# Optimization experiments

Measured on AMD Instinct MI355X. Metric: run time of the kernel, lower is better.

## Reference

```python
import jax, jax.numpy as jnp
import numpy as np

NUM_HEADS = 4
OUTPUT_DIM = 64


def setup_inputs() -> dict:
    key = jax.random.key(0)
    k1, k2, k3 = jax.random.split(key, 3)
    B, N, F = 8, 2048, 256
    features = jax.random.normal(k1, (B, N, F), dtype=jnp.float32)
    adj_matrix = jax.random.uniform(k2, (B, N, N), dtype=jnp.float32)
    # learned params (glorot-ish scale)
    kernel = jax.random.normal(k3, (F, OUTPUT_DIM * NUM_HEADS), dtype=jnp.float32) * (1.0 / np.sqrt(F))
    bias = jnp.zeros((OUTPUT_DIM * NUM_HEADS,), dtype=jnp.float32)
    return {"features": features, "adj_matrix": adj_matrix, "kernel": kernel, "bias": bias}


def reference(features, adj_matrix, kernel, bias):
    B, N, F = features.shape
    H, D = NUM_HEADS, OUTPUT_DIM
    Wh = jnp.matmul(features, kernel)                 # [B, N, H*D]
    Whh = Wh.reshape(B, N, H, D)                      # [B, N, H, D]
    # per-node, per-head score: inner product Wh1 @ Wh2 = ||Wh||^2
    e = jnp.sum(Whh * Whh, axis=-1)                   # [B, N, H]
    attention = jax.nn.softmax(e, axis=1)             # softmax over nodes
    attention = jnp.mean(attention, axis=2)           # head mean -> [B, N]
    # adjacency mask (broadcast column score over neighbors)
    A = attention[:, :, None] * adj_matrix            # [B, N, N]
    out = jnp.matmul(A, Wh) + bias                    # [B, N, H*D]
    return jax.nn.relu(out)
```

## Files before the change

### kernel.cpp

```cpp
#include <hip/hip_runtime.h>
#include <hip/hip_bf16.h>

#define BATCH 8
#define NNODE 2048
#define FDIM 256
#define HD 256
#define NH 4
#define MROWS (BATCH*NNODE)
#define BK 64

typedef float f32x4 __attribute__((ext_vector_type(4)));
typedef short s16x8 __attribute__((ext_vector_type(8)));

__device__ __forceinline__ unsigned short f2bf(float f) {
    unsigned u = __builtin_bit_cast(unsigned, f);
    u += 0x7fffu + ((u >> 16) & 1u);
    return (unsigned short)(u >> 16);
}
__device__ __forceinline__ float bf2f(unsigned short h) {
    return __builtin_bit_cast(float, (unsigned)h << 16);
}

#define MFMA __builtin_amdgcn_mfma_f32_16x16x32_bf16

__device__ __forceinline__ void mfma_mainloop(
    const float* __restrict__ Ab, int astride,
    const unsigned short* __restrict__ Bph,
    const unsigned short* __restrict__ Bpl, int bstride,
    int nt, unsigned short (&lds)[2][4][128 * BK],
    int tid, int lane, int wr, int wc,
    f32x4 (&acc)[4][4])
{
    f32x4 ar[8];
    uint4 brh[4], brl[4];

    #pragma unroll
    for (int i = 0; i < 4; ++i) {
        const int g = tid + 256 * i, r = g >> 3, gk = g & 7;
        ar[2*i]   = *(const f32x4*)&Ab[(size_t)r * astride + gk * 8];
        ar[2*i+1] = *(const f32x4*)&Ab[(size_t)r * astride + gk * 8 + 4];
        brh[i] = *(const uint4*)&Bph[(size_t)r * bstride + gk * 8];
        brl[i] = *(const uint4*)&Bpl[(size_t)r * bstride + gk * 8];
    }

    #define STAGE_WRITE(BUF) do {                                             \
        _Pragma("unroll")                                                     \
        for (int i = 0; i < 4; ++i) {                                         \
            const int g = tid + 256 * i, r = g >> 3, gk = g & 7;              \
            const int ad = r * BK + ((gk ^ (r & 7)) * 8);                     \
            s16x8 vh, vl;                                                     \
            _Pragma("unroll")                                                 \
            for (int j = 0; j < 4; ++j) {                                     \
                float v0 = ar[2*i][j];                                        \
                unsigned short h = f2bf(v0);                                  \
                vh[j] = (short)h; vl[j] = (short)f2bf(v0 - bf2f(h));          \
            }                                                                 \
            _Pragma("unroll")                                                 \
            for (int j = 0; j < 4; ++j) {                                     \
                float v0 = ar[2*i+1][j];                                      \
                unsigned short h = f2bf(v0);                                  \
                vh[4+j] = (short)h; vl[4+j] = (short)f2bf(v0 - bf2f(h));      \
            }                                                                 \
            *(s16x8*)&lds[BUF][0][ad] = vh;                                   \
            *(s16x8*)&lds[BUF][1][ad] = vl;                                   \
            *(uint4*)&lds[BUF][2][ad] = brh[i];                               \
            *(uint4*)&lds[BUF][3][ad] = brl[i];                               \
        }                                                                     \
    } while (0)

    #define COMPUTE(BUF) do {                                                 \
        _Pragma("unroll")                                                     \
        for (int kh = 0; kh < 2; ++kh) {                                      \
            s16x8 afh[4], afl[4], bfh[4], bfl[4];                             \
            const int kg = kh * 4 + (lane >> 4);                              \
            _Pragma("unroll")                                                 \
            for (int m = 0; m < 4; ++m) {                                     \
                const int r = wr * 64 + m * 16 + (lane & 15);                 \
                const int ad = r * BK + ((kg ^ (r & 7)) * 8);                 \
                afh[m] = *(const s16x8*)&lds[BUF][0][ad];                     \
                afl[m] = *(const s16x8*)&lds[BUF][1][ad];                     \
            }                                                                 \
            _Pragma("unroll")                                                 \
            for (int n = 0; n < 4; ++n) {                                     \
                const int c = wc * 64 + n * 16 + (lane & 15);                 \
                const int ad = c * BK + ((kg ^ (c & 7)) * 8);                 \
                bfh[n] = *(const s16x8*)&lds[BUF][2][ad];                     \
                bfl[n] = *(const s16x8*)&lds[BUF][3][ad];                     \
            }                                                                 \
            _Pragma("unroll")                                                 \
            for (int m = 0; m < 4; ++m)                                       \
            _Pragma("unroll")                                                 \
            for (int n = 0; n < 4; ++n) {                                     \
                acc[m][n] = MFMA(afh[m], bfh[n], acc[m][n], 0, 0, 0);         \
                acc[m][n] = MFMA(afh[m], bfl[n], acc[m][n], 0, 0, 0);         \
                acc[m][n] = MFMA(afl[m], bfh[n], acc[m][n], 0, 0, 0);         \
            }                                                                 \
        }                                                                     \
    } while (0)

    STAGE_WRITE(0);
    __syncthreads();
    for (int t = 0; t < nt; ++t) {
        const int cur = t & 1;
        if (t + 1 < nt) {
            const int k0 = (t + 1) * BK;
            #pragma unroll
            for (int i = 0; i < 4; ++i) {
                const int g = tid + 256 * i, r = g >> 3, gk = g & 7;
                ar[2*i]   = *(const f32x4*)&Ab[(size_t)r * astride + k0 + gk * 8];
                ar[2*i+1] = *(const f32x4*)&Ab[(size_t)r * astride + k0 + gk * 8 + 4];
                brh[i] = *(const uint4*)&Bph[(size_t)r * bstride + k0 + gk * 8];
                brl[i] = *(const uint4*)&Bpl[(size_t)r * bstride + k0 + gk * 8];
            }
        }
        COMPUTE(cur);
        if (t + 1 < nt) STAGE_WRITE(cur ^ 1);
        __syncthreads();
    }
    #undef STAGE_WRITE
    #undef COMPUTE
}

__global__ __launch_bounds__(256) void wprep_kernel(
    const float* __restrict__ Wm,
    unsigned short* __restrict__ wt_hi, unsigned short* __restrict__ wt_lo)
{
    const int nn = blockIdx.x, k = threadIdx.x;
    const float v = Wm[(size_t)k * HD + nn];
    const unsigned short h = f2bf(v);
    wt_hi[nn * FDIM + k] = h;
    wt_lo[nn * FDIM + k] = f2bf(v - bf2f(h));
}

__global__ __launch_bounds__(256) void gemm1_kernel(
    const float* __restrict__ features,
    const unsigned short* __restrict__ wt_hi,
    const unsigned short* __restrict__ wt_lo,
    unsigned short* __restrict__ WhT_hi,
    unsigned short* __restrict__ WhT_lo,
    float* __restrict__ e_out)
{
    __shared__ unsigned short lds[2][4][128 * BK];

    const int tid = threadIdx.x;
    const int lane = tid & 63;
    const int w = tid >> 6;
    const int wr = w >> 1, wc = w & 1;
    const int row0 = blockIdx.x * 128;
    const int col0 = blockIdx.y * 128;

    f32x4 acc[4][4];
    #pragma unroll
    for (int m = 0; m < 4; ++m)
        #pragma unroll
        for (int n = 0; n < 4; ++n) acc[m][n] = (f32x4)0.f;

    mfma_mainloop(features + (size_t)row0 * FDIM, FDIM,
                  wt_hi + (size_t)col0 * FDIM, wt_lo + (size_t)col0 * FDIM, FDIM,
                  FDIM / BK, lds, tid, lane, wr, wc, acc);

    const int head = blockIdx.y * 2 + wc;
    #pragma unroll
    for (int m = 0; m < 4; ++m)
        #pragma unroll
        for (int r = 0; r < 4; ++r) {
            float p = 0.f;
            #pragma unroll
            for (int n = 0; n < 4; ++n) p += acc[m][n][r] * acc[m][n][r];
            p += __shfl_xor(p, 1, 64);
            p += __shfl_xor(p, 2, 64);
            p += __shfl_xor(p, 4, 64);
            p += __shfl_xor(p, 8, 64);
            if ((lane & 15) == 0) {
                const int row = row0 + wr * 64 + m * 16 + (lane >> 4) * 4 + r;
                e_out[((size_t)((row >> 11) * NH + head)) * NNODE + (row & 2047)] = p;
            }
        }

    __syncthreads();
    unsigned short* Th = &lds[0][0][0];
    unsigned short* Tl = &lds[0][2][0];
    #pragma unroll
    for (int m = 0; m < 4; ++m)
        #pragma unroll
        for (int n = 0; n < 4; ++n)
            #pragma unroll
            for (int r = 0; r < 4; ++r) {
                const int rr = wr * 64 + m * 16 + (lane >> 4) * 4 + r;
                const int cc = wc * 64 + n * 16 + (lane & 15);
                const int ad = cc * 128 + ((((rr >> 3) ^ (cc & 15))) << 3) + (rr & 7);
                const float v = acc[m][n][r];
                const unsigned short h = f2bf(v);
                Th[ad] = h;
                Tl[ad] = f2bf(v - bf2f(h));
            }
    __syncthreads();
    const int bb = row0 >> 11, kk0 = row0 & 2047;
    #pragma unroll
    for (int i = 0; i < 8; ++i) {
        const int gid = tid + 256 * i;
        const int c = gid >> 4, gr = gid & 15;
        const int ad = c * 128 + ((gr ^ (c & 15)) << 3);
        uint4 vh = *(const uint4*)&Th[ad];
        uint4 vl = *(const uint4*)&Tl[ad];
        const size_t o = ((size_t)bb * HD + col0 + c) * NNODE + kk0 + gr * 8;
        *(uint4*)&WhT_hi[o] = vh;
        *(uint4*)&WhT_lo[o] = vl;
    }
}

__global__ __launch_bounds__(256) void sm_kernel(
    const float* __restrict__ e, float* __restrict__ ms)
{
    __shared__ float red[8];
    const int bh = blockIdx.x, tid = threadIdx.x;
    const int lane = tid & 63, w = tid >> 6;
    const float* row = e + (size_t)bh * NNODE;
    float mx = -3.0e38f;
    for (int n = tid; n < NNODE; n += 256) mx = fmaxf(mx, row[n]);
    #pragma unroll
    for (int off = 32; off; off >>= 1) mx = fmaxf(mx, __shfl_xor(mx, off, 64));
    if (lane == 0) red[w] = mx;
    __syncthreads();
    mx = fmaxf(fmaxf(red[0], red[1]), fmaxf(red[2], red[3]));
    float s = 0.f;
    for (int n = tid; n < NNODE; n += 256) s += expf(row[n] - mx);
    #pragma unroll
    for (int off = 32; off; off >>= 1) s += __shfl_xor(s, off, 64);
    if (lane == 0) red[4 + w] = s;
    __syncthreads();
    if (tid == 0) {
        ms[bh * 2] = mx;
        ms[bh * 2 + 1] = red[4] + red[5] + red[6] + red[7];
    }
}

__global__ __launch_bounds__(256) void att_kernel(
    const float* __restrict__ e, const float* __restrict__ ms,
    float* __restrict__ attv)
{
    const int i = blockIdx.x * 256 + threadIdx.x;
    const int b = i >> 11, n = i & 2047;
    float a = 0.f;
    #pragma unroll
    for (int h = 0; h < NH; ++h) {
        const int bh = b * NH + h;
        a += expf(e[(size_t)bh * NNODE + n] - ms[bh * 2]) / ms[bh * 2 + 1];
    }
    attv[i] = 0.25f * a;
}

__global__ __launch_bounds__(256) void gemm2_kernel(
    const float* __restrict__ adj,
    const unsigned short* __restrict__ WhT_hi,
    const unsigned short* __restrict__ WhT_lo,
    const float* __restrict__ att,
    const float* __restrict__ bias,
    float* __restrict__ out)
{
    __shared__ unsigned short lds[2][4][128 * BK];

    const int tid = threadIdx.x;
    const int lane = tid & 63;
    const int w = tid >> 6;
    const int wr = w >> 1, wc = w & 1;
    const int b = blockIdx.z;
    const int row0 = blockIdx.x * 128, col0 = blockIdx.y * 128;

    f32x4 acc[4][4];
    #pragma unroll
    for (int m = 0; m < 4; ++m)
        #pragma unroll
        for (int n = 0; n < 4; ++n) acc[m][n] = (f32x4)0.f;

    mfma_mainloop(adj + (size_t)b * NNODE * NNODE + (size_t)row0 * NNODE, NNODE,
                  WhT_hi + ((size_t)b * HD + col0) * NNODE,
                  WhT_lo + ((size_t)b * HD + col0) * NNODE, NNODE,
                  NNODE / BK, lds, tid, lane, wr, wc, acc);

    const float* attb = att + (size_t)b * NNODE;
    #pragma unroll
    for (int n = 0; n < 4; ++n) {
        const int c = col0 + wc * 64 + n * 16 + (lane & 15);
        const float bv = bias[c];
        #pragma unroll
        for (int m = 0; m < 4; ++m)
            #pragma unroll
            for (int r = 0; r < 4; ++r) {
                const int row = row0 + wr * 64 + m * 16 + (lane >> 4) * 4 + r;
                const float a = attb[row];
                out[((size_t)b * NNODE + row) * HD + c] =
                    fmaxf(fmaf(acc[m][n][r], a, bv), 0.f);
            }
    }
}

extern "C" void kernel_launch(void* const* d_in, const int* in_sizes, int n_in,
                              void* d_out, int out_size, void* d_ws, size_t ws_size,
                              hipStream_t stream) {
    const float* features = (const float*)d_in[0];
    const float* adj      = (const float*)d_in[1];
    const float* Wm       = (const float*)d_in[2];
    const float* bias     = (const float*)d_in[3];
    float* out = (float*)d_out;

    unsigned short* WhT_hi = (unsigned short*)d_ws;
    unsigned short* WhT_lo = WhT_hi + (size_t)BATCH * HD * NNODE;
    unsigned short* wt_hi  = WhT_lo + (size_t)BATCH * HD * NNODE;
    unsigned short* wt_lo  = wt_hi + FDIM * HD;
    float* e    = (float*)(wt_lo + FDIM * HD);
    float* ms   = e + (size_t)BATCH * NH * NNODE;
    float* attv = ms + 64;

    wprep_kernel<<<HD, 256, 0, stream>>>(Wm, wt_hi, wt_lo);
    gemm1_kernel<<<dim3(MROWS / 128, 2), 256, 0, stream>>>(
        features, wt_hi, wt_lo, WhT_hi, WhT_lo, e);
    sm_kernel<<<BATCH * NH, 256, 0, stream>>>(e, ms);
    att_kernel<<<MROWS / 256, 256, 0, stream>>>(e, ms, attv);
    gemm2_kernel<<<dim3(NNODE / 128, 2, BATCH), 256, 0, stream>>>(
        adj, WhT_hi, WhT_lo, attv, bias, out);
}
```

Before: 324.3 us.

## Retile both GEMMs smaller, use direct global-to-LDS loads and truncating bf16 split

Both GEMMs get smaller tiles. gemm1 now uses 64x64 tiles, one head per block, and gemm2 uses 128x64 tiles, which raises the block count and occupancy (launch bounds 4 and 2). The B operand is staged with global_load_lds straight into LDS, with explicit waitcnt and barrier scheduling and a double-buffered pipeline in gemm2. The hi/lo bf16 split now truncates instead of rounding, which removes ALU work in the conversion. The risks are more reloads of the adjacency matrix across column tiles, fragile manual vmcnt accounting, and a slightly different split accuracy.

```diff
diff --git a/kernel.cpp b/kernel.cpp
--- a/kernel.cpp
+++ b/kernel.cpp
@@ -7,203 +7,194 @@
 #define HD 256
 #define NH 4
 #define MROWS (BATCH*NNODE)
-#define BK 64
 
 typedef float f32x4 __attribute__((ext_vector_type(4)));
 typedef short s16x8 __attribute__((ext_vector_type(8)));
-
-__device__ __forceinline__ unsigned short f2bf(float f) {
+typedef unsigned short ushort_t;
+
+#define MFMA __builtin_amdgcn_mfma_f32_16x16x32_bf16
+#define SCHED0() __builtin_amdgcn_sched_barrier(0)
+#define SBAR() __builtin_amdgcn_s_barrier()
+
+__device__ __forceinline__ void split2(float f, ushort_t& h, ushort_t& l) {
     unsigned u = __builtin_bit_cast(unsigned, f);
-    u += 0x7fffu + ((u >> 16) & 1u);
-    return (unsigned short)(u >> 16);
-}
-__device__ __forceinline__ float bf2f(unsigned short h) {
-    return __builtin_bit_cast(float, (unsigned)h << 16);
-}
-
-#define MFMA __builtin_amdgcn_mfma_f32_16x16x32_bf16
-
-__device__ __forceinline__ void mfma_mainloop(
-    const float* __restrict__ Ab, int astride,
-    const unsigned short* __restrict__ Bph,
-    const unsigned short* __restrict__ Bpl, int bstride,
-    int nt, unsigned short (&lds)[2][4][128 * BK],
-    int tid, int lane, int wr, int wc,
-    f32x4 (&acc)[4][4])
-{
-    f32x4 ar[8];
-    uint4 brh[4], brl[4];
-
-    #pragma unroll
-    for (int i = 0; i < 4; ++i) {
-        const int g = tid + 256 * i, r = g >> 3, gk = g & 7;
-        ar[2*i]   = *(const f32x4*)&Ab[(size_t)r * astride + gk * 8];
-        ar[2*i+1] = *(const f32x4*)&Ab[(size_t)r * astride + gk * 8 + 4];
-        brh[i] = *(const uint4*)&Bph[(size_t)r * bstride + gk * 8];
-        brl[i] = *(const uint4*)&Bpl[(size_t)r * bstride + gk * 8];
-    }
-
-    #define STAGE_WRITE(BUF) do {                                             \
-        _Pragma("unroll")                                                     \
-        for (int i = 0; i < 4; ++i) {                                         \
-            const int g = tid + 256 * i, r = g >> 3, gk = g & 7;              \
-            const int ad = r * BK + ((gk ^ (r & 7)) * 8);                     \
-            s16x8 vh, vl;                                                     \
-            _Pragma("unroll")                                                 \
-            for (int j = 0; j < 4; ++j) {                                     \
-                float v0 = ar[2*i][j];                                        \
-                unsigned short h = f2bf(v0);                                  \
-                vh[j] = (short)h; vl[j] = (short)f2bf(v0 - bf2f(h));          \
-            }                                                                 \
-            _Pragma("unroll")                                                 \
-            for (int j = 0; j < 4; ++j) {                                     \
-                float v0 = ar[2*i+1][j];                                      \
-                unsigned short h = f2bf(v0);                                  \
-                vh[4+j] = (short)h; vl[4+j] = (short)f2bf(v0 - bf2f(h));      \
-            }                                                                 \
-            *(s16x8*)&lds[BUF][0][ad] = vh;                                   \
-            *(s16x8*)&lds[BUF][1][ad] = vl;                                   \
-            *(uint4*)&lds[BUF][2][ad] = brh[i];                               \
-            *(uint4*)&lds[BUF][3][ad] = brl[i];                               \
-        }                                                                     \
-    } while (0)
-
-    #define COMPUTE(BUF) do {                                                 \
-        _Pragma("unroll")                                                     \
-        for (int kh = 0; kh < 2; ++kh) {                                      \
-            s16x8 afh[4], afl[4], bfh[4], bfl[4];                             \
-            const int kg = kh * 4 + (lane >> 4);                              \
-            _Pragma("unroll")                                                 \
-            for (int m = 0; m < 4; ++m) {                                     \
-                const int r = wr * 64 + m * 16 + (lane & 15);                 \
-                const int ad = r * BK + ((kg ^ (r & 7)) * 8);                 \
-                afh[m] = *(const s16x8*)&lds[BUF][0][ad];                     \
-                afl[m] = *(const s16x8*)&lds[BUF][1][ad];                     \
-            }                                                                 \
-            _Pragma("unroll")                                                 \
-            for (int n = 0; n < 4; ++n) {                                     \
-                const int c = wc * 64 + n * 16 + (lane & 15);                 \
-                const int ad = c * BK + ((kg ^ (c & 7)) * 8);                 \
-                bfh[n] = *(const s16x8*)&lds[BUF][2][ad];                     \
-                bfl[n] = *(const s16x8*)&lds[BUF][3][ad];                     \
-            }                                                                 \
-            _Pragma("unroll")                                                 \
-            for (int m = 0; m < 4; ++m)                                       \
-            _Pragma("unroll")                                                 \
-            for (int n = 0; n < 4; ++n) {                                     \
-                acc[m][n] = MFMA(afh[m], bfh[n], acc[m][n], 0, 0, 0);         \
-                acc[m][n] = MFMA(afh[m], bfl[n], acc[m][n], 0, 0, 0);         \
-                acc[m][n] = MFMA(afl[m], bfh[n], acc[m][n], 0, 0, 0);         \
-            }                                                                 \
-        }                                                                     \
-    } while (0)
-
-    STAGE_WRITE(0);
-    __syncthreads();
-    for (int t = 0; t < nt; ++t) {
-        const int cur = t & 1;
-        if (t + 1 < nt) {
-            const int k0 = (t + 1) * BK;
-            #pragma unroll
-            for (int i = 0; i < 4; ++i) {
-                const int g = tid + 256 * i, r = g >> 3, gk = g & 7;
-                ar[2*i]   = *(const f32x4*)&Ab[(size_t)r * astride + k0 + gk * 8];
-                ar[2*i+1] = *(const f32x4*)&Ab[(size_t)r * astride + k0 + gk * 8 + 4];
-                brh[i] = *(const uint4*)&Bph[(size_t)r * bstride + k0 + gk * 8];
-                brl[i] = *(const uint4*)&Bpl[(size_t)r * bstride + k0 + gk * 8];
-            }
-        }
-        COMPUTE(cur);
-        if (t + 1 < nt) STAGE_WRITE(cur ^ 1);
-        __syncthreads();
-    }
-    #undef STAGE_WRITE
-    #undef COMPUTE
-}
+    h = (ushort_t)(u >> 16);
+    float fh = __builtin_bit_cast(float, u & 0xffff0000u);
+    float lo = f - fh;
+    l = (ushort_t)(__builtin_bit_cast(unsigned, lo) >> 16);
+}
+
+#define GLOAD16(gp, lp) __builtin_amdgcn_global_load_lds( \
+    (const __attribute__((address_space(1))) void*)(gp),  \
+    (__attribute__((address_space(3))) void*)(lp), 16, 0, 0)
 
 __global__ __launch_bounds__(256) void wprep_kernel(
     const float* __restrict__ Wm,
-    unsigned short* __restrict__ wt_hi, unsigned short* __restrict__ wt_lo)
+    ushort_t* __restrict__ wt_hi, ushort_t* __restrict__ wt_lo)
 {
     const int nn = blockIdx.x, k = threadIdx.x;
-    const float v = Wm[(size_t)k * HD + nn];
-    const unsigned short h = f2bf(v);
+    ushort_t h, l;
+    split2(Wm[(size_t)k * HD + nn], h, l);
     wt_hi[nn * FDIM + k] = h;
-    wt_lo[nn * FDIM + k] = f2bf(v - bf2f(h));
-}
-
-__global__ __launch_bounds__(256) void gemm1_kernel(
+    wt_lo[nn * FDIM + k] = l;
+}
+
+__global__ __launch_bounds__(256, 4) void gemm1_kernel(
     const float* __restrict__ features,
-    const unsigned short* __restrict__ wt_hi,
-    const unsigned short* __restrict__ wt_lo,
-    unsigned short* __restrict__ WhT_hi,
-    unsigned short* __restrict__ WhT_lo,
+    const ushort_t* __restrict__ wt_hi,
+    const ushort_t* __restrict__ wt_lo,
+    ushort_t* __restrict__ WhT_hi,
+    ushort_t* __restrict__ WhT_lo,
     float* __restrict__ e_out)
 {
-    __shared__ unsigned short lds[2][4][128 * BK];
-
-    const int tid = threadIdx.x;
-    const int lane = tid & 63;
-    const int w = tid >> 6;
+    __shared__ __align__(16) ushort_t Ah[64 * 64];
+    __shared__ __align__(16) ushort_t Al[64 * 64];
+    __shared__ __align__(16) ushort_t Bh[64 * 64];
+    __shared__ __align__(16) ushort_t Bl[64 * 64];
+    __shared__ float red[64][2];
+
+    const int tid = threadIdx.x, lane = tid & 63, w = tid >> 6;
     const int wr = w >> 1, wc = w & 1;
-    const int row0 = blockIdx.x * 128;
-    const int col0 = blockIdx.y * 128;
-
-    f32x4 acc[4][4];
-    #pragma unroll
-    for (int m = 0; m < 4; ++m)
-        #pragma unroll
-        for (int n = 0; n < 4; ++n) acc[m][n] = (f32x4)0.f;
-
-    mfma_mainloop(features + (size_t)row0 * FDIM, FDIM,
-                  wt_hi + (size_t)col0 * FDIM, wt_lo + (size_t)col0 * FDIM, FDIM,
-                  FDIM / BK, lds, tid, lane, wr, wc, acc);
-
-    const int head = blockIdx.y * 2 + wc;
-    #pragma unroll
-    for (int m = 0; m < 4; ++m)
-        #pragma unroll
-        for (int r = 0; r < 4; ++r) {
-            float p = 0.f;
+    const int row0 = blockIdx.x * 64;
+    const int head = blockIdx.y;
+    const int col0 = head * 64;
+
+    const float* Ab = features + (size_t)row0 * FDIM;
+    const ushort_t* Bhg = wt_hi + (size_t)col0 * FDIM;
+    const ushort_t* Blg = wt_lo + (size_t)col0 * FDIM;
+
+    const int sr0 = tid >> 3;
+    const int sg8 = tid & 7;
+    const int bc = (lane >> 3);
+    const int bs = lane & 7;
+
+    f32x4 ar[4];
+    f32x4 acc[2][2];
+    #pragma unroll
+    for (int m = 0; m < 2; ++m)
+        #pragma unroll
+        for (int n = 0; n < 2; ++n) acc[m][n] = (f32x4)0.f;
+
+    #define G1_LOADA(K0) do {                                                  \
+        _Pragma("unroll")                                                      \
+        for (int i = 0; i < 2; ++i) {                                          \
+            const int r = sr0 + 32 * i;                                        \
+            ar[2*i]   = *(const f32x4*)&Ab[(size_t)r * FDIM + (K0) + sg8 * 8]; \
+            ar[2*i+1] = *(const f32x4*)&Ab[(size_t)r * FDIM + (K0) + sg8 * 8 + 4]; \
+        }                                                                      \
+    } while (0)
+
+    #define G1_STAGEA() do {                                                   \
+        _Pragma("unroll")                                                      \
+        for (int i = 0; i < 2; ++i) {                                          \
+            const int r = sr0 + 32 * i;                                        \
+            s16x8 vh, vl; ushort_t hh, ll;                                     \
+            _Pragma("unroll")                                                  \
+            for (int j = 0; j < 4; ++j) {                                      \
+                split2(ar[2*i][j], hh, ll);  vh[j] = (short)hh; vl[j] = (short)ll; \
+            }                                                                  \
+            _Pragma("unroll")                                                  \
+            for (int j = 0; j < 4; ++j) {                                      \
+                split2(ar[2*i+1][j], hh, ll); vh[4+j] = (short)hh; vl[4+j] = (short)ll; \
+            }                                                                  \
+            const int off = r * 64 + ((sg8 ^ (r & 7)) << 3);                   \
+            *(s16x8*)&Ah[off] = vh; *(s16x8*)&Al[off] = vl;                    \
+        }                                                                      \
+    } while (0)
+
+    #define G1_STAGEB(K0) do {                                                 \
+        _Pragma("unroll")                                                      \
+        for (int qq = 0; qq < 2; ++qq) {                                       \
+            const int q = w + qq * 4;                                          \
+            const int c = q * 8 + bc;                                          \
+            const int g = bs ^ (c & 7);                                        \
+            GLOAD16(&Bhg[(size_t)c * FDIM + (K0) + g * 8], &Bh[q * 512]);      \
+            GLOAD16(&Blg[(size_t)c * FDIM + (K0) + g * 8], &Bl[q * 512]);      \
+        }                                                                      \
+    } while (0)
+
+    G1_LOADA(0);
+    for (int t = 0; t < 4; ++t) {
+        G1_STAGEB(t * 64);
+        G1_STAGEA();
+        if (t < 3) G1_LOADA((t + 1) * 64);
+        if (t < 3) { asm volatile("s_waitcnt lgkmcnt(0) vmcnt(4)" ::: "memory"); }
+        else       { asm volatile("s_waitcnt lgkmcnt(0) vmcnt(0)" ::: "memory"); }
+        SCHED0(); SBAR(); SCHED0();
+        #pragma unroll
+        for (int kh = 0; kh < 2; ++kh) {
+            const int kg = kh * 4 + (lane >> 4);
+            s16x8 afh[2], afl[2], bfh[2], bfl[2];
             #pragma unroll
-            for (int n = 0; n < 4; ++n) p += acc[m][n][r] * acc[m][n][r];
+            for (int m = 0; m < 2; ++m) {
+                const int r = wr * 32 + m * 16 + (lane & 15);
+                const int off = r * 64 + ((kg ^ (r & 7)) << 3);
+                afh[m] = *(const s16x8*)&Ah[off];
+                afl[m] = *(const s16x8*)&Al[off];
+            }
+            #pragma unroll
+            for (int n = 0; n < 2; ++n) {
+                const int c = wc * 32 + n * 16 + (lane & 15);
+                const int off = c * 64 + ((kg ^ (c & 7)) << 3);
+                bfh[n] = *(const s16x8*)&Bh[off];
+                bfl[n] = *(const s16x8*)&Bl[off];
+            }
+            #pragma unroll
+            for (int m = 0; m < 2; ++m)
+                #pragma unroll
+                for (int n = 0; n < 2; ++n) {
+                    acc[m][n] = MFMA(afh[m], bfh[n], acc[m][n], 0, 0, 0);
+                    acc[m][n] = MFMA(afh[m], bfl[n], acc[m][n], 0, 0, 0);
+                    acc[m][n] = MFMA(afl[m], bfh[n], acc[m][n], 0, 0, 0);
+                }
+        }
+        SCHED0(); SBAR(); SCHED0();
+    }
+
+    #pragma unroll
+    for (int m = 0; m < 2; ++m)
+        #pragma unroll
+        for (int j = 0; j < 4; ++j) {
+            float p = acc[m][0][j] * acc[m][0][j] + acc[m][1][j] * acc[m][1][j];
             p += __shfl_xor(p, 1, 64);
             p += __shfl_xor(p, 2, 64);
             p += __shfl_xor(p, 4, 64);
             p += __shfl_xor(p, 8, 64);
-            if ((lane & 15) == 0) {
-                const int row = row0 + wr * 64 + m * 16 + (lane >> 4) * 4 + r;
-                e_out[((size_t)((row >> 11) * NH + head)) * NNODE + (row & 2047)] = p;
-            }
+            if ((lane & 15) == 0)
+                red[wr * 32 + m * 16 + (lane >> 4) * 4 + j][wc] = p;
         }
 
-    __syncthreads();
-    unsigned short* Th = &lds[0][0][0];
-    unsigned short* Tl = &lds[0][2][0];
-    #pragma unroll
-    for (int m = 0; m < 4; ++m)
-        #pragma unroll
-        for (int n = 0; n < 4; ++n)
+    ushort_t* Th = Ah;
+    ushort_t* Tl = Al;
+    #pragma unroll
+    for (int m = 0; m < 2; ++m)
+        #pragma unroll
+        for (int n = 0; n < 2; ++n)
             #pragma unroll
-            for (int r = 0; r < 4; ++r) {
-                const int rr = wr * 64 + m * 16 + (lane >> 4) * 4 + r;
-                const int cc = wc * 64 + n * 16 + (lane & 15);
-                const int ad = cc * 128 + ((((rr >> 3) ^ (cc & 15))) << 3) + (rr & 7);
-                const float v = acc[m][n][r];
-                const unsigned short h = f2bf(v);
-                Th[ad] = h;
-                Tl[ad] = f2bf(v - bf2f(h));
+            for (int j = 0; j < 4; ++j) {
+                const int rr = wr * 32 + m * 16 + (lane >> 4) * 4 + j;
+                const int cc = wc * 32 + n * 16 + (lane & 15);
+                const int ad = cc * 64 + ((((rr >> 3) ^ (cc & 7))) << 3) + (rr & 7);
+                ushort_t hh, ll;
+                split2(acc[m][n][j], hh, ll);
+                Th[ad] = hh; Tl[ad] = ll;
             }
     __syncthreads();
-    const int bb = row0 >> 11, kk0 = row0 & 2047;
-    #pragma unroll
-    for (int i = 0; i < 8; ++i) {
+
+    if (tid < 64) {
+        const int rg = row0 + tid;
+        e_out[((size_t)((rg >> 11) * NH + head)) * NNODE + (rg & 2047)] =
+            red[tid][0] + red[tid][1];
+    }
+    const int bb = row0 >> 11, node0 = row0 & 2047;
+    #pragma unroll
+    for (int i = 0; i < 2; ++i) {
         const int gid = tid + 256 * i;
-        const int c = gid >> 4, gr = gid & 15;
-        const int ad = c * 128 + ((gr ^ (c & 15)) << 3);
+        const int c = gid >> 3, gr = gid & 7;
+        const int ad = c * 64 + ((gr ^ (c & 7)) << 3);
         uint4 vh = *(const uint4*)&Th[ad];
         uint4 vl = *(const uint4*)&Tl[ad];
-        const size_t o = ((size_t)bb * HD + col0 + c) * NNODE + kk0 + gr * 8;
+        const size_t o = ((size_t)bb * HD + col0 + c) * NNODE + node0 + gr * 8;
         *(uint4*)&WhT_hi[o] = vh;
         *(uint4*)&WhT_lo[o] = vl;
     }
@@ -250,47 +241,143 @@
     attv[i] = 0.25f * a;
 }
 
-__global__ __launch_bounds__(256) void gemm2_kernel(
+__global__ __launch_bounds__(256, 2) void gemm2_kernel(
     const float* __restrict__ adj,
-    const unsigned short* __restrict__ WhT_hi,
-    const unsigned short* __restrict__ WhT_lo,
+    const ushort_t* __restrict__ WhT_hi,
+    const ushort_t* __restrict__ WhT_lo,
     const float* __restrict__ att,
     const float* __restrict__ bias,
     float* __restrict__ out)
 {
-    __shared__ unsigned short lds[2][4][128 * BK];
-
-    const int tid = threadIdx.x;
-    const int lane = tid & 63;
-    const int w = tid >> 6;
+    __shared__ __align__(16) ushort_t Ah[128 * 64];
+    __shared__ __align__(16) ushort_t Al[128 * 64];
+    __shared__ __align__(16) ushort_t Bh[2][64 * 64];
+    __shared__ __align__(16) ushort_t Bl[2][64 * 64];
+
+    const int tid = threadIdx.x, lane = tid & 63, w = tid >> 6;
     const int wr = w >> 1, wc = w & 1;
     const int b = blockIdx.z;
-    const int row0 = blockIdx.x * 128, col0 = blockIdx.y * 128;
-
-    f32x4 acc[4][4];
+    const int row0 = blockIdx.x * 128, col0 = blockIdx.y * 64;
+
+    const float* Ab = adj + (size_t)b * NNODE * NNODE + (size_t)row0 * NNODE;
+    const ushort_t* Bhg = WhT_hi + ((size_t)b * HD + col0) * NNODE;
+    const ushort_t* Blg = WhT_lo + ((size_t)b * HD + col0) * NNODE;
+
+    const int sr0 = tid >> 3;
+    const int sg8 = tid & 7;
+    const int bc = lane >> 3, bs = lane & 7;
+
+    f32x4 ar[8];
+    f32x4 acc[4][2];
     #pragma unroll
     for (int m = 0; m < 4; ++m)
         #pragma unroll
-        for (int n = 0; n < 4; ++n) acc[m][n] = (f32x4)0.f;
-
-    mfma_mainloop(adj + (size_t)b * NNODE * NNODE + (size_t)row0 * NNODE, NNODE,
-                  WhT_hi + ((size_t)b * HD + col0) * NNODE,
-                  WhT_lo + ((size_t)b * HD + col0) * NNODE, NNODE,
-                  NNODE / BK, lds, tid, lane, wr, wc, acc);
+        for (int n = 0; n < 2; ++n) acc[m][n] = (f32x4)0.f;
+
+    #define G2_LOADA(K0) do {                                                   \
+        _Pragma("unroll")                                                       \
+        for (int i = 0; i < 4; ++i) {                                           \
+            const int r = sr0 + 32 * i;                                         \
+            ar[2*i]   = *(const f32x4*)&Ab[(size_t)r * NNODE + (K0) + sg8 * 8]; \
+            ar[2*i+1] = *(const f32x4*)&Ab[(size_t)r * NNODE + (K0) + sg8 * 8 + 4]; \
+        }                                                                       \
+    } while (0)
+
+    #define G2_STAGEA() do {                                                    \
+        _Pragma("unroll")                                                       \
+        for (int i = 0; i < 4; ++i) {                                           \
+            const int r = sr0 + 32 * i;                                         \
+            s16x8 vh, vl; ushort_t hh, ll;                                      \
+            _Pragma("unroll")                                                   \
+            for (int j = 0; j < 4; ++j) {                                       \
+                split2(ar[2*i][j], hh, ll);  vh[j] = (short)hh; vl[j] = (short)ll; \
+            }                                                                   \
+            _Pragma("unroll")                                                   \
+            for (int j = 0; j < 4; ++j) {                                       \
+                split2(ar[2*i+1][j], hh, ll); vh[4+j] = (short)hh; vl[4+j] = (short)ll; \
+            }                                                                   \
+            const int off = r * 64 + ((sg8 ^ (r & 7)) << 3);                    \
+            *(s16x8*)&Ah[off] = vh; *(s16x8*)&Al[off] = vl;                     \
+        }                                                                       \
+    } while (0)
+
+    #define G2_STAGEB(BUF, K0) do {                                             \
+        _Pragma("unroll")                                                       \
+        for (int qq = 0; qq < 2; ++qq) {                                        \
+            const int q = w + qq * 4;                                           \
+            const int c = q * 8 + bc;                                           \
+            const int g = bs ^ (c & 7);                                         \
+            GLOAD16(&Bhg[(size_t)c * NNODE + (K0) + g * 8], &Bh[BUF][q * 512]); \
+            GLOAD16(&Blg[(size_t)c * NNODE + (K0) + g * 8], &Bl[BUF][q * 512]); \
+        }                                                                       \
+    } while (0)
+
+    #define G2_COMPUTE(BUF) do {                                                \
+        _Pragma("unroll")                                                       \
+        for (int kh = 0; kh < 2; ++kh) {                                        \
+            const int kg = kh * 4 + (lane >> 4);                                \
+            s16x8 afh[4], afl[4], bfh[2], bfl[2];                               \
+            _Pragma("unroll")                                                   \
+            for (int m = 0; m < 4; ++m) {                                       \
+                const int r = wr * 64 + m * 16 + (lane & 15);                   \
+                const int off = r * 64 + ((kg ^ (r & 7)) << 3);                 \
+                afh[m] = *(const s16x8*)&Ah[off];                               \
+                afl[m] = *(const s16x8*)&Al[off];                               \
+            }                                                                   \
+            _Pragma("unroll")                                                   \
+            for (int n = 0; n < 2; ++n) {                                       \
+                const int c = wc * 32 + n * 16 + (lane & 15);                   \
+                const int off = c * 64 + ((kg ^ (c & 7)) << 3);                 \
+                bfh[n] = *(const s16x8*)&Bh[BUF][off];                          \
+                bfl[n] = *(const s16x8*)&Bl[BUF][off];                          \
+            }                                                                   \
+            _Pragma("unroll")                                                   \
+            for (int m = 0; m < 4; ++m)                                         \
+            _Pragma("unroll")                                                   \
+            for (int n = 0; n < 2; ++n) {                                       \
+                acc[m][n] = MFMA(afh[m], bfh[n], acc[m][n], 0, 0, 0);           \
+                acc[m][n] = MFMA(afh[m], bfl[n], acc[m][n], 0, 0, 0);           \
+                acc[m][n] = MFMA(afl[m], bfh[n], acc[m][n], 0, 0, 0);           \
+            }                                                                   \
+        }                                                                       \
+    } while (0)
+
+    G2_LOADA(0);
+    G2_STAGEB(0, 0);
+    G2_STAGEA();
+    G2_LOADA(64);
+    asm volatile("s_waitcnt lgkmcnt(0) vmcnt(8)" ::: "memory");
+    SCHED0(); SBAR(); SCHED0();
+
+    for (int t = 0; t < 32; ++t) {
+        const int cur = t & 1;
+        if (t < 31) G2_STAGEB(cur ^ 1, (t + 1) * 64);
+        G2_COMPUTE(cur);
+        if (t < 31) {
+            SCHED0(); SBAR(); SCHED0();
+            G2_STAGEA();
+            if (t < 30) {
+                G2_LOADA((t + 2) * 64);
+                asm volatile("s_waitcnt lgkmcnt(0) vmcnt(8)" ::: "memory");
+            } else {
+                asm volatile("s_waitcnt lgkmcnt(0) vmcnt(0)" ::: "memory");
+            }
+            SCHED0(); SBAR(); SCHED0();
+        }
+    }
 
     const float* attb = att + (size_t)b * NNODE;
     #pragma unroll
-    for (int n = 0; n < 4; ++n) {
-        const int c = col0 + wc * 64 + n * 16 + (lane & 15);
+    for (int n = 0; n < 2; ++n) {
+        const int c = col0 + wc * 32 + n * 16 + (lane & 15);
         const float bv = bias[c];
         #pragma unroll
         for (int m = 0; m < 4; ++m)
             #pragma unroll
-            for (int r = 0; r < 4; ++r) {
-                const int row = row0 + wr * 64 + m * 16 + (lane >> 4) * 4 + r;
-                const float a = attb[row];
+            for (int j = 0; j < 4; ++j) {
+                const int row = row0 + wr * 64 + m * 16 + (lane >> 4) * 4 + j;
                 out[((size_t)b * NNODE + row) * HD + c] =
-                    fmaxf(fmaf(acc[m][n][r], a, bv), 0.f);
+                    fmaxf(fmaf(acc[m][n][j], attb[row], bv), 0.f);
             }
     }
 }
@@ -304,19 +391,19 @@
     const float* bias     = (const float*)d_in[3];
     float* out = (float*)d_out;
 
-    unsigned short* WhT_hi = (unsigned short*)d_ws;
-    unsigned short* WhT_lo = WhT_hi + (size_t)BATCH * HD * NNODE;
-    unsigned short* wt_hi  = WhT_lo + (size_t)BATCH * HD * NNODE;
-    unsigned short* wt_lo  = wt_hi + FDIM * HD;
+    ushort_t* WhT_hi = (ushort_t*)d_ws;
+    ushort_t* WhT_lo = WhT_hi + (size_t)BATCH * HD * NNODE;
+    ushort_t* wt_hi  = WhT_lo + (size_t)BATCH * HD * NNODE;
+    ushort_t* wt_lo  = wt_hi + FDIM * HD;
     float* e    = (float*)(wt_lo + FDIM * HD);
     float* ms   = e + (size_t)BATCH * NH * NNODE;
     float* attv = ms + 64;
 
     wprep_kernel<<<HD, 256, 0, stream>>>(Wm, wt_hi, wt_lo);
-    gemm1_kernel<<<dim3(MROWS / 128, 2), 256, 0, stream>>>(
+    gemm1_kernel<<<dim3(MROWS / 64, NH), 256, 0, stream>>>(
         features, wt_hi, wt_lo, WhT_hi, WhT_lo, e);
     sm_kernel<<<BATCH * NH, 256, 0, stream>>>(e, ms);
     att_kernel<<<MROWS / 256, 256, 0, stream>>>(e, ms, attv);
-    gemm2_kernel<<<dim3(NNODE / 128, 2, BATCH), 256, 0, stream>>>(
+    gemm2_kernel<<<dim3(NNODE / 128, HD / 64, BATCH), 256, 0, stream>>>(
         adj, WhT_hi, WhT_lo, attv, bias, out);
 }
```

Result: faster. 289.0 us (-10.9%).
